# Performance work log

Measured on AMD Instinct MI355X. Metric: run time of the kernel, lower is better.

Reference implementation:

```python
import jax, jax.numpy as jnp
import numpy as np

N, C, H, W = 4, 64, 64, 64
K = 3


def _unfold(x, k):
    """torch F.unfold with padding k//2: [n,c,h,w] -> [n, c*k*k, h*w].
    Feature ordering matches torch: index = c*k*k + i*k + j."""
    p = k // 2
    n, c, h, w = x.shape
    xp = jnp.pad(x, ((0, 0), (0, 0), (p, p), (p, p)))
    patches = jnp.stack(
        [xp[:, :, i:i + h, j:j + w] for i in range(k) for j in range(k)], axis=2
    )  # [n, c, k*k, h, w]
    return patches.reshape(n, c * k * k, h * w)


def _mask_vec(c, k):
    # causal patch mask from __init__: zero out center-and-right of middle row and all rows below
    m = np.ones((c, k, k), np.float32)
    m[:, k // 2, k // 2:] = 0
    m[:, k // 2 + 1:, :] = 0
    return jnp.asarray(m.reshape(1, c * k * k, 1))


def setup_inputs() -> dict:
    key = jax.random.key(0)
    k1, k2 = jax.random.split(key)
    y_hat = jax.random.normal(k1, (N, C, H, W), dtype=jnp.float32)
    y_prob = jax.random.uniform(k2, (N, 1, H, W), dtype=jnp.float32)
    return {"y_hat": y_hat, "y_prob": y_prob}


def reference(y_hat, y_prob):
    k = K
    n, c, h, w = y_hat.shape
    L = h * w
    mask = _mask_vec(c, k)

    u = _unfold(y_hat, k) * mask                              # [n, c*k*k, L]
    u = u / jnp.maximum(jnp.linalg.norm(u, axis=1, keepdims=True), 1e-12)
    R = jnp.einsum('nfl,nfm->nlm', u, u)                      # [n, L, L] cosine sims

    # eval path: keep strictly-upper triangle (causal: l < m)
    row = jnp.arange(L)[:, None]
    col = jnp.arange(L)[None, :]
    R = jnp.where(col > row, R, 0.0)

    R_star = jnp.max(R, axis=1)                               # [n, L]
    arg = jnp.argmax(R, axis=1).astype(jnp.int32)             # [n, L]

    y_unf = _unfold(y_hat, k)                                 # [n, c*k*k, L]
    ref_unfold = jnp.take_along_axis(y_unf, arg[:, None, :], axis=2)

    prob_unf = y_prob.reshape(n, -1, L)                       # 1x1 unfold
    U_unf = jnp.take_along_axis(prob_unf, arg[:, None, :], axis=2)

    S = R_star.reshape(n, 1, h, w)
    U = U_unf.reshape(n, -1, h, w)

    # eval-mode position-0 overrides
    S = S.at[:, :, 0, 0].set(1e-8)
    U = U.at[:, :, 0, 0].set(1e-8)
    ref_unfold = ref_unfold.at[:, :, 0].set(0.0)
    arg = arg.at[:, 0].set(-1)

    S = jnp.clip(S, 1e-8, 1.0)
    U = jnp.clip(U, 1e-8, 1.0)
    return S, U, ref_unfold, arg
```

## Files before the change

### kernel.cpp

```cpp
#include <hip/hip_runtime.h>
#include <stdint.h>

#define Nn 4
#define Cc 64
#define LL 4096
#define KK 256
#define TRI2 528

typedef _Float16 half8 __attribute__((ext_vector_type(8)));
typedef float f32x16 __attribute__((ext_vector_type(16)));
typedef float f4a __attribute__((ext_vector_type(4), aligned(4)));
typedef unsigned short ushort8v __attribute__((ext_vector_type(8)));

__device__ __forceinline__ unsigned f2ord(float f) {
    unsigned u = __float_as_uint(f);
    return u ^ ((u & 0x80000000u) ? 0xFFFFFFFFu : 0x80000000u);
}
__device__ __forceinline__ float ord2f(unsigned o) {
    unsigned u = (o & 0x80000000u) ? (o ^ 0x80000000u) : ~o;
    return __uint_as_float(u);
}
__device__ __forceinline__ unsigned short h2u(_Float16 h) {
    union { _Float16 f; unsigned short u; } x; x.f = h; return x.u;
}

__global__ __launch_bounds__(256) void build_v(const float* __restrict__ yhat,
                                               unsigned short* __restrict__ VhT,
                                               unsigned short* __restrict__ VlT,
                                               unsigned long long* __restrict__ best) {
    int blk = blockIdx.x;
    int xcd = blk & 7;
    int n = xcd >> 1;
    int i64 = (blk >> 3) + (xcd & 1) * 128;
    int tid = threadIdx.x;
    if (tid < 16) best[(size_t)n * LL + i64 * 16 + tid] = 0ull;

    int cg = tid & 15;
    int l = i64 * 16 + (tid >> 4);
    int y = l >> 6, x = l & 63;
    const float* src = yhat + (size_t)n * (Cc * LL);

    float vals[16];
    float sumsq = 0.f;
#pragma unroll
    for (int ci = 0; ci < 4; ++ci) {
        const float* p = src + (cg * 4 + ci) * LL;
        float t0 = (y > 0 && x > 0)  ? p[l - 65] : 0.f;
        float t1 = (y > 0)           ? p[l - 64] : 0.f;
        float t2 = (y > 0 && x < 63) ? p[l - 63] : 0.f;
        float t3 = (x > 0)           ? p[l - 1]  : 0.f;
        vals[ci * 4 + 0] = t0; vals[ci * 4 + 1] = t1;
        vals[ci * 4 + 2] = t2; vals[ci * 4 + 3] = t3;
        sumsq += t0 * t0 + t1 * t1 + t2 * t2 + t3 * t3;
    }
    sumsq += __shfl_xor(sumsq, 1, 64);
    sumsq += __shfl_xor(sumsq, 2, 64);
    sumsq += __shfl_xor(sumsq, 4, 64);
    sumsq += __shfl_xor(sumsq, 8, 64);
    float inv = 1.f / fmaxf(sqrtf(sumsq), 1e-12f);

    size_t pk = ((((size_t)n * 128 + (l >> 5)) * 16 + cg) << 9) + (l & 31) * 8;
    unsigned short* dh = VhT + pk;
    unsigned short* dl = VlT + pk;
    ushort8v hA, hB, lA, lB;
#pragma unroll
    for (int kk = 0; kk < 16; ++kk) {
        float v = vals[kk] * inv;
        _Float16 h = (fabsf(v) < 6.1035e-5f) ? (_Float16)0 : (_Float16)v;
        _Float16 lo = (_Float16)((v - (float)h) * 2048.0f);
        unsigned short hu = h2u(h * (_Float16)2048.0f);
        unsigned short lu = h2u(lo);
        if (kk < 8) { hA[kk] = hu; lA[kk] = lu; }
        else        { hB[kk - 8] = hu; lB[kk - 8] = lu; }
    }
    *(ushort8v*)(dh)       = hA;
    *(ushort8v*)(dh + 256) = hB;
    *(ushort8v*)(dl)       = lA;
    *(ushort8v*)(dl + 256) = lB;
}

__global__ __launch_bounds__(512) void simmax(const unsigned short* __restrict__ Vh,
                                              const unsigned short* __restrict__ Vl,
                                              unsigned long long* __restrict__ best) {
    __shared__ __align__(16) unsigned short S[16384];

    int bx = blockIdx.x;
    int xcd = bx & 7, idx = bx >> 3;
    int n = xcd >> 1;
    int t = (xcd & 1) * 264 + idx;

    int J = (int)((sqrtf(32.f * (float)t + 4.f) - 2.f) * 0.0625f);
    while (8 * (J + 1) * (J + 1) + 2 * (J + 1) <= t) ++J;
    while (8 * J * J + 2 * J > t) --J;
    int r = t - (8 * J * J + 2 * J);
    int i, j;
    if (r < 16 * J) {
        int I = r >> 4, inner = r & 15;
        i = 4 * I + (inner & 3);
        j = 4 * J + (inner >> 2);
    } else {
        int rr = r - 16 * J;
        int dj = (rr >= 6) ? 3 : (rr >= 3) ? 2 : (rr >= 1) ? 1 : 0;
        int di = rr - ((dj * (dj + 1)) >> 1);
        i = 4 * J + di;
        j = 4 * J + dj;
    }
    int l0 = i * 128, m0 = j * 128;

    int tid = threadIdx.x;
    int w = __builtin_amdgcn_readfirstlane(tid >> 6);
    int lane = tid & 63;
    int r5 = lane & 31, h5 = lane >> 5;
    int rw = (w & 1) * 64;
    int cw = (w >> 1) * 32;
    bool skip = (i == j) && (rw == 64) && (cw < 64);

    const unsigned short* VhB = Vh + (size_t)n * (LL * KK);
    const unsigned short* VlB = Vl + (size_t)n * (LL * KK);

    int aRow0 = l0 >> 5;
    int bRow0 = m0 >> 5;

    int laneElem = lane * 8;

    const unsigned short* gsrcA[2];
    int lslotA[2];
#pragma unroll
    for (int q = 0; q < 2; ++q) {
        int rb = w >> 1, lo = w & 1;
        gsrcA[q] = (lo ? VlB : VhB) + ((size_t)((aRow0 + rb) * 16 + q) << 9) + laneElem;
        lslotA[q] = (2 * w + q) * 512;
    }
    const unsigned short* pBh = VhB + ((size_t)((bRow0 + (w >> 1)) * 16) << 9) + laneElem;
    const unsigned short* pBl = VlB + ((size_t)((bRow0 + (w >> 1)) * 16) << 9) + laneElem;

    int arb = (w & 1) * 2;

    f32x16 acc[2];
#pragma unroll
    for (int r2 = 0; r2 < 2; ++r2) acc[r2] = (f32x16)0.f;

#define GLDSA(KQ, BN)                                                             \
    do {                                                                          \
        _Pragma("unroll")                                                         \
        for (int q = 0; q < 2; ++q)                                               \
            __builtin_amdgcn_global_load_lds(                                     \
                (const __attribute__((address_space(1))) void*)(gsrcA[q] + (size_t)(KQ) * 1024), \
                (__attribute__((address_space(3))) void*)(S + (BN) * 8192 + lslotA[q]), 16, 0, 0); \
    } while (0)

#define MFMA_SET(AL, AH, BH, BL)                                                  \
    do {                                                                          \
        __builtin_amdgcn_s_setprio(1);                                            \
        _Pragma("unroll")                                                         \
        for (int kc = 0; kc < 2; ++kc)                                            \
            _Pragma("unroll")                                                     \
            for (int r2 = 0; r2 < 2; ++r2)                                        \
                acc[r2] = __builtin_amdgcn_mfma_f32_32x32x16_f16((AL)[r2][kc], (BH)[kc], acc[r2], 0, 0, 0); \
        _Pragma("unroll")                                                         \
        for (int kc = 0; kc < 2; ++kc)                                            \
            _Pragma("unroll")                                                     \
            for (int r2 = 0; r2 < 2; ++r2)                                        \
                acc[r2] = __builtin_amdgcn_mfma_f32_32x32x16_f16((AH)[r2][kc], (BL)[kc], acc[r2], 0, 0, 0); \
        _Pragma("unroll")                                                         \
        for (int kc = 0; kc < 2; ++kc)                                            \
            _Pragma("unroll")                                                     \
            for (int r2 = 0; r2 < 2; ++r2)                                        \
                acc[r2] = __builtin_amdgcn_mfma_f32_32x32x16_f16((AH)[r2][kc], (BH)[kc], acc[r2], 0, 0, 0); \
        __builtin_amdgcn_s_setprio(0);                                            \
    } while (0)

    half8 bhP[2], blP[2], bhQ[2], blQ[2];

    GLDSA(0, 0);
    __builtin_amdgcn_sched_barrier(0);
    if (!skip) {
        bhP[0] = *(const half8*)(pBh);        bhP[1] = *(const half8*)(pBh + 512);
        blP[0] = *(const half8*)(pBl);        blP[1] = *(const half8*)(pBl + 512);
    }

#pragma unroll
    for (int kq = 0; kq < 8; ++kq) {
        const int cur = (kq & 1) * 8192;
        const bool even = (kq & 1) == 0;

        if (skip) { asm volatile("s_waitcnt lgkmcnt(0) vmcnt(0)" ::: "memory"); }
        else      { asm volatile("s_waitcnt lgkmcnt(0) vmcnt(4)" ::: "memory"); }
        __builtin_amdgcn_s_barrier();
        __builtin_amdgcn_sched_barrier(0);

        if (kq < 7) {
            GLDSA(kq + 1, (kq + 1) & 1);
            __builtin_amdgcn_sched_barrier(0);
            if (!skip) {
                const unsigned short* nh = pBh + (size_t)(kq + 1) * 1024;
                const unsigned short* nl = pBl + (size_t)(kq + 1) * 1024;
                if (even) {
                    bhQ[0] = *(const half8*)(nh);       bhQ[1] = *(const half8*)(nh + 512);
                    blQ[0] = *(const half8*)(nl);       blQ[1] = *(const half8*)(nl + 512);
                } else {
                    bhP[0] = *(const half8*)(nh);       bhP[1] = *(const half8*)(nh + 512);
                    blP[0] = *(const half8*)(nl);       blP[1] = *(const half8*)(nl + 512);
                }
            }
        }

        if (!skip) {
            half8 al[2][2], ah[2][2];
#pragma unroll
            for (int kc = 0; kc < 2; ++kc)
#pragma unroll
                for (int r2 = 0; r2 < 2; ++r2) {
                    al[r2][kc] = *(const half8*)(S + cur + (((arb + r2) * 2 + 1) * 2 + kc) * 512 + laneElem);
                    ah[r2][kc] = *(const half8*)(S + cur + (((arb + r2) * 2) * 2 + kc) * 512 + laneElem);
                }
            if (even) MFMA_SET(al, ah, bhP, blP);
            else      MFMA_SET(al, ah, bhQ, blQ);
        }
    }
#undef GLDSA
#undef MFMA_SET

    if (skip) return;
    unsigned long long* bb = best + (size_t)n * LL;
    const float s = 1.f / 4194304.f;
    {
        int m = m0 + cw + r5;
        unsigned long long key = 0ull;
#pragma unroll
        for (int r2 = 0; r2 < 2; ++r2)
#pragma unroll
            for (int g = 0; g < 16; ++g) {
                int l = l0 + rw + r2 * 32 + (g & 3) + 8 * (g >> 2) + 4 * h5;
                if (l < m) {
                    float v = acc[r2][g] * s;
                    unsigned long long k2 =
                        ((unsigned long long)f2ord(v) << 32) |
                        (unsigned long long)(0xFFFFFFFFu - (unsigned)l);
                    key = (k2 > key) ? k2 : key;
                }
            }
        unsigned long long o = __shfl_xor(key, 32, 64);
        key = (o > key) ? o : key;
        if (h5 == 0 && key != 0ull) atomicMax(bb + m, key);
    }
}

__global__ __launch_bounds__(256) void writeout(const float* __restrict__ yhat,
                                                const float* __restrict__ yprob,
                                                const unsigned long long* __restrict__ best,
                                                float* __restrict__ out) {
    int blk = blockIdx.x;
    int xcd = blk & 7;
    int n = xcd >> 1;
    int idx = (blk >> 3) + (xcd & 1) * 512;
    int mb = idx >> 4;
    int fc = idx & 15;
    int tid = threadIdx.x;
    int mm = tid & 63;
    int fs = tid >> 6;
    int c = fc * 4 + fs;
    int m = mb * 64 + mm;

    unsigned long long key = best[(size_t)n * LL + m];
    unsigned l = 0xFFFFFFFFu - (unsigned)(key & 0xFFFFFFFFull);
    float val = ord2f((unsigned)(key >> 32));
    bool zero = (m == 0);
    if (zero) l = 0;
    int ly = (int)(l >> 6), lx = (int)(l & 63);

    float* Sout = out;
    float* Uout = out + 16384;
    float* Rout = out + 32768;
    float* Aout = out + 9469952;

    if (fc == 0 && fs == 0) {
        float S = zero ? 1e-8f : fminf(fmaxf(val, 1e-8f), 1.0f);
        float U = zero ? 1e-8f : fminf(fmaxf(yprob[(size_t)n * LL + l], 1e-8f), 1.0f);
        Sout[(size_t)n * LL + m] = S;
        Uout[(size_t)n * LL + m] = U;
        Aout[(size_t)n * LL + m] = zero ? -1.0f : (float)l;
    }

    const float* src = yhat + (size_t)n * (Cc * LL);
    const float* plane = src + (size_t)c * LL;
    float* dst = Rout + (size_t)n * (576 * LL) + m;
    bool fast = (!zero) && (lx >= 1) && (lx <= 61);
#pragma unroll
    for (int r3 = 0; r3 < 3; ++r3) {
        int yy = ly + r3 - 1;
        bool rowok = (!zero) && (yy >= 0) && (yy < 64);
        float t0 = 0.f, t1 = 0.f, t2 = 0.f;
        if (rowok) {
            if (fast) {
                f4a v = *(const f4a*)(plane + yy * 64 + lx - 1);
                t0 = v.x; t1 = v.y; t2 = v.z;
            } else {
                if (lx > 0)  t0 = plane[yy * 64 + lx - 1];
                t1 = plane[yy * 64 + lx];
                if (lx < 63) t2 = plane[yy * 64 + lx + 1];
            }
        }
        size_t f = (size_t)(c * 9 + r3 * 3) * LL;
        __builtin_nontemporal_store(t0, dst + f);
        __builtin_nontemporal_store(t1, dst + f + LL);
        __builtin_nontemporal_store(t2, dst + f + 2 * (size_t)LL);
    }
}

extern "C" void kernel_launch(void* const* d_in, const int* in_sizes, int n_in,
                              void* d_out, int out_size, void* d_ws, size_t ws_size,
                              hipStream_t stream) {
    const float* yhat  = (const float*)d_in[0];
    const float* yprob = (const float*)d_in[1];
    float* out = (float*)d_out;

    unsigned short* VhT = (unsigned short*)d_ws;
    unsigned short* VlT = (unsigned short*)((char*)d_ws + 8388608);
    unsigned long long* best =
        (unsigned long long*)((char*)d_ws + 16777216);

    build_v<<<1024, 256, 0, stream>>>(yhat, VhT, VlT, best);
    simmax<<<Nn * TRI2, 512, 0, stream>>>(VhT, VlT, best);
    writeout<<<4096, 256, 0, stream>>>(yhat, yprob, best, out);
}
```

Before: 150.4 us.

## Stage B operand through LDS via async global_load_lds alongside A

The B-side fragments of the similarity GEMM were loaded per wave straight from global memory into registers, with a partial vmcnt wait. They are now staged into shared memory together with the A-side tiles using async global-to-LDS loads, with a doubled LDS buffer and a full waitcnt barrier each phase. This cuts register pressure and duplicated global traffic across waves that share B rows. In exchange it doubles LDS usage, which may lower occupancy, and adds a stricter wait on every pipeline step.

```diff
diff --git a/kernel.cpp b/kernel.cpp
--- a/kernel.cpp
+++ b/kernel.cpp
@@ -22,6 +22,12 @@
 }
 __device__ __forceinline__ unsigned short h2u(_Float16 h) {
     union { _Float16 f; unsigned short u; } x; x.f = h; return x.u;
+}
+
+__device__ __forceinline__ void pipe_barrier() {
+    asm volatile("s_waitcnt lgkmcnt(0) vmcnt(0)" ::: "memory");
+    __builtin_amdgcn_s_barrier();
+    __builtin_amdgcn_sched_barrier(0);
 }
 
 __global__ __launch_bounds__(256) void build_v(const float* __restrict__ yhat,
@@ -82,7 +88,7 @@
 __global__ __launch_bounds__(512) void simmax(const unsigned short* __restrict__ Vh,
                                               const unsigned short* __restrict__ Vl,
                                               unsigned long long* __restrict__ best) {
-    __shared__ __align__(16) unsigned short S[16384];
+    __shared__ __align__(16) unsigned short S[32768];
 
     int bx = blockIdx.x;
     int xcd = bx & 7, idx = bx >> 3;
@@ -123,103 +129,74 @@
 
     int laneElem = lane * 8;
 
-    const unsigned short* gsrcA[2];
-    int lslotA[2];
-#pragma unroll
-    for (int q = 0; q < 2; ++q) {
-        int rb = w >> 1, lo = w & 1;
-        gsrcA[q] = (lo ? VlB : VhB) + ((size_t)((aRow0 + rb) * 16 + q) << 9) + laneElem;
-        lslotA[q] = (2 * w + q) * 512;
-    }
-    const unsigned short* pBh = VhB + ((size_t)((bRow0 + (w >> 1)) * 16) << 9) + laneElem;
-    const unsigned short* pBl = VlB + ((size_t)((bRow0 + (w >> 1)) * 16) << 9) + laneElem;
+    const unsigned short* gsrc[4];
+    int lslot[4];
+#pragma unroll
+    for (int q = 0; q < 4; ++q) {
+        int c = w * 4 + q;
+        int side = c >> 4, rb = (c >> 2) & 3, lo = (c >> 1) & 1, kc = c & 1;
+        int rowblk = (side ? bRow0 : aRow0) + rb;
+        gsrc[q] = (lo ? VlB : VhB) + (((size_t)(rowblk * 16) + kc) << 9) + laneElem;
+        lslot[q] = c * 512;
+    }
 
     int arb = (w & 1) * 2;
+    int brb = (w >> 1);
 
     f32x16 acc[2];
 #pragma unroll
     for (int r2 = 0; r2 < 2; ++r2) acc[r2] = (f32x16)0.f;
 
-#define GLDSA(KQ, BN)                                                             \
+#define GLDS(PH, BN)                                                              \
     do {                                                                          \
         _Pragma("unroll")                                                         \
-        for (int q = 0; q < 2; ++q)                                               \
+        for (int q = 0; q < 4; ++q)                                               \
             __builtin_amdgcn_global_load_lds(                                     \
-                (const __attribute__((address_space(1))) void*)(gsrcA[q] + (size_t)(KQ) * 1024), \
-                (__attribute__((address_space(3))) void*)(S + (BN) * 8192 + lslotA[q]), 16, 0, 0); \
+                (const __attribute__((address_space(1))) void*)(gsrc[q] + (size_t)(PH) * 1024), \
+                (__attribute__((address_space(3))) void*)(S + (BN) * 16384 + lslot[q]), 16, 0, 0); \
     } while (0)
 
-#define MFMA_SET(AL, AH, BH, BL)                                                  \
-    do {                                                                          \
-        __builtin_amdgcn_s_setprio(1);                                            \
-        _Pragma("unroll")                                                         \
-        for (int kc = 0; kc < 2; ++kc)                                            \
-            _Pragma("unroll")                                                     \
-            for (int r2 = 0; r2 < 2; ++r2)                                        \
-                acc[r2] = __builtin_amdgcn_mfma_f32_32x32x16_f16((AL)[r2][kc], (BH)[kc], acc[r2], 0, 0, 0); \
-        _Pragma("unroll")                                                         \
-        for (int kc = 0; kc < 2; ++kc)                                            \
-            _Pragma("unroll")                                                     \
-            for (int r2 = 0; r2 < 2; ++r2)                                        \
-                acc[r2] = __builtin_amdgcn_mfma_f32_32x32x16_f16((AH)[r2][kc], (BL)[kc], acc[r2], 0, 0, 0); \
-        _Pragma("unroll")                                                         \
-        for (int kc = 0; kc < 2; ++kc)                                            \
-            _Pragma("unroll")                                                     \
-            for (int r2 = 0; r2 < 2; ++r2)                                        \
-                acc[r2] = __builtin_amdgcn_mfma_f32_32x32x16_f16((AH)[r2][kc], (BH)[kc], acc[r2], 0, 0, 0); \
-        __builtin_amdgcn_s_setprio(0);                                            \
-    } while (0)
-
-    half8 bhP[2], blP[2], bhQ[2], blQ[2];
-
-    GLDSA(0, 0);
-    __builtin_amdgcn_sched_barrier(0);
-    if (!skip) {
-        bhP[0] = *(const half8*)(pBh);        bhP[1] = *(const half8*)(pBh + 512);
-        blP[0] = *(const half8*)(pBl);        blP[1] = *(const half8*)(pBl + 512);
-    }
-
-#pragma unroll
-    for (int kq = 0; kq < 8; ++kq) {
-        const int cur = (kq & 1) * 8192;
-        const bool even = (kq & 1) == 0;
-
-        if (skip) { asm volatile("s_waitcnt lgkmcnt(0) vmcnt(0)" ::: "memory"); }
-        else      { asm volatile("s_waitcnt lgkmcnt(0) vmcnt(4)" ::: "memory"); }
-        __builtin_amdgcn_s_barrier();
-        __builtin_amdgcn_sched_barrier(0);
-
-        if (kq < 7) {
-            GLDSA(kq + 1, (kq + 1) & 1);
-            __builtin_amdgcn_sched_barrier(0);
-            if (!skip) {
-                const unsigned short* nh = pBh + (size_t)(kq + 1) * 1024;
-                const unsigned short* nl = pBl + (size_t)(kq + 1) * 1024;
-                if (even) {
-                    bhQ[0] = *(const half8*)(nh);       bhQ[1] = *(const half8*)(nh + 512);
-                    blQ[0] = *(const half8*)(nl);       blQ[1] = *(const half8*)(nl + 512);
-                } else {
-                    bhP[0] = *(const half8*)(nh);       bhP[1] = *(const half8*)(nh + 512);
-                    blP[0] = *(const half8*)(nl);       blP[1] = *(const half8*)(nl + 512);
+    GLDS(0, 0);
+
+#pragma unroll
+    for (int p = 0; p < 8; ++p) {
+        const int cur = (p & 1) * 16384;
+
+        pipe_barrier();
+        if (p < 7) GLDS(p + 1, (p + 1) & 1);
+
+        if (!skip) {
+            half8 al[2][2], ah[2][2], bh[2], bl[2];
+#pragma unroll
+            for (int kc = 0; kc < 2; ++kc) {
+#pragma unroll
+                for (int r2 = 0; r2 < 2; ++r2) {
+                    al[r2][kc] = *(const half8*)(S + cur + ((arb + r2) * 4 + 2 + kc) * 512 + laneElem);
+                    ah[r2][kc] = *(const half8*)(S + cur + ((arb + r2) * 4 + kc) * 512 + laneElem);
                 }
+                bh[kc] = *(const half8*)(S + cur + (16 + brb * 4 + kc) * 512 + laneElem);
+                bl[kc] = *(const half8*)(S + cur + (16 + brb * 4 + 2 + kc) * 512 + laneElem);
             }
+            __builtin_amdgcn_s_setprio(1);
+#pragma unroll
+            for (int kc = 0; kc < 2; ++kc)
+#pragma unroll
+                for (int r2 = 0; r2 < 2; ++r2)
+                    acc[r2] = __builtin_amdgcn_mfma_f32_32x32x16_f16(al[r2][kc], bh[kc], acc[r2], 0, 0, 0);
+#pragma unroll
+            for (int kc = 0; kc < 2; ++kc)
+#pragma unroll
+                for (int r2 = 0; r2 < 2; ++r2)
+                    acc[r2] = __builtin_amdgcn_mfma_f32_32x32x16_f16(ah[r2][kc], bl[kc], acc[r2], 0, 0, 0);
+#pragma unroll
+            for (int kc = 0; kc < 2; ++kc)
+#pragma unroll
+                for (int r2 = 0; r2 < 2; ++r2)
+                    acc[r2] = __builtin_amdgcn_mfma_f32_32x32x16_f16(ah[r2][kc], bh[kc], acc[r2], 0, 0, 0);
+            __builtin_amdgcn_s_setprio(0);
         }
-
-        if (!skip) {
-            half8 al[2][2], ah[2][2];
-#pragma unroll
-            for (int kc = 0; kc < 2; ++kc)
-#pragma unroll
-                for (int r2 = 0; r2 < 2; ++r2) {
-                    al[r2][kc] = *(const half8*)(S + cur + (((arb + r2) * 2 + 1) * 2 + kc) * 512 + laneElem);
-                    ah[r2][kc] = *(const half8*)(S + cur + (((arb + r2) * 2) * 2 + kc) * 512 + laneElem);
-                }
-            if (even) MFMA_SET(al, ah, bhP, blP);
-            else      MFMA_SET(al, ah, bhQ, blQ);
-        }
-    }
-#undef GLDSA
-#undef MFMA_SET
+    }
+#undef GLDS
 
     if (skip) return;
     unsigned long long* bb = best + (size_t)n * LL;
```

Result: no change. 148.9 us (-1.0%).
